# Kernel optimization log

Hardware: AMD Instinct MI355X
Metric: run time of the kernel (lower is better)

## Reference

```python
import jax, jax.numpy as jnp
import numpy as np

B, T, I, H = 64, 512, 512, 1024

def _xavier(key, shape):
    fan_in, fan_out = shape
    limit = float(np.sqrt(6.0 / (fan_in + fan_out)))
    return jax.random.uniform(key, shape, jnp.float32, -limit, limit)

def setup_inputs() -> dict:
    key = jax.random.key(0)
    ks = jax.random.split(key, 9)
    inp = {
        'x': jax.random.normal(ks[0], (B, T, I), jnp.float32),
        'U_inputgate': _xavier(ks[1], (I, H)),
        'V_inputgate': _xavier(ks[2], (H, H)),
        'bias_inputgate': jnp.zeros((H,), jnp.float32),
        'U_forget': _xavier(ks[3], (I, H)),
        'V_forget': _xavier(ks[4], (H, H)),
        'bias_forget': jnp.zeros((H,), jnp.float32),
        'U_tilded': _xavier(ks[5], (I, H)),
        'V_tilded': _xavier(ks[6], (H, H)),
        'bias_tilded': jnp.zeros((H,), jnp.float32),
        'U_output': _xavier(ks[7], (I, H)),
        'V_output': _xavier(ks[8], (H, H)),
        'bias_output': jnp.zeros((H,), jnp.float32),
    }
    return inp

def reference(x, U_inputgate, V_inputgate, bias_inputgate,
              U_forget, V_forget, bias_forget,
              U_tilded, V_tilded, bias_tilded,
              U_output, V_output, bias_output):
    batch = x.shape[0]
    hidden = V_inputgate.shape[0]
    # Precompute input projections for all timesteps (fused gate GEMM):
    # concat U's -> one [I, 4H] GEMM over the whole sequence.
    U = jnp.concatenate([U_inputgate, U_forget, U_tilded, U_output], axis=1)  # [I, 4H]
    V = jnp.concatenate([V_inputgate, V_forget, V_tilded, V_output], axis=1)  # [H, 4H]
    b = jnp.concatenate([bias_inputgate, bias_forget, bias_tilded, bias_output])  # [4H]
    xU = jnp.einsum('bti,ig->btg', x, U) + b  # [B, T, 4H]

    def step(carry, xu_t):
        h, c = carry
        g = xu_t + h @ V  # [B, 4H]
        i_g = jax.nn.sigmoid(g[:, :hidden])
        f_g = jax.nn.sigmoid(g[:, hidden:2 * hidden])
        c_t = jnp.tanh(g[:, 2 * hidden:3 * hidden])
        o_g = jax.nn.sigmoid(g[:, 3 * hidden:])
        c_new = i_g * c_t + f_g * c
        h_new = o_g * jnp.tanh(c_new)
        return (h_new, c_new), None

    h0 = jnp.zeros((batch, hidden), x.dtype)
    c0 = jnp.zeros((batch, hidden), x.dtype)
    (h_t, c_t), _ = jax.lax.scan(step, (h0, c0), jnp.swapaxes(xU, 0, 1))
    return (h_t, c_t)
```

## Files before the change

### kernel.cpp

```cpp
#include <hip/hip_runtime.h>
#include <hip/hip_bf16.h>
#include <cstdio>
#include <cstdint>

#define BB 64
#define TT 512
#define II 512
#define HH 1024
#define G4H 4096
#define TC 256

typedef __attribute__((ext_vector_type(8))) short short8b;
typedef __attribute__((ext_vector_type(4))) float f32x4;
typedef unsigned long long ull;

union U16 { uint4 u; short8b s; };

#define AT_LD32(p)   __hip_atomic_load((p), __ATOMIC_RELAXED, __HIP_MEMORY_SCOPE_AGENT)
#define AT_LD64(p)   __hip_atomic_load((p), __ATOMIC_RELAXED, __HIP_MEMORY_SCOPE_AGENT)
#define AT_ST32(p,v) __hip_atomic_store((p), (v), __ATOMIC_RELAXED, __HIP_MEMORY_SCOPE_AGENT)
#define AT_ST64(p,v) __hip_atomic_store((p), (v), __ATOMIC_RELAXED, __HIP_MEMORY_SCOPE_AGENT)

__device__ __forceinline__ ushort f2bf(float f) {
    union { float f; unsigned u; } x; x.f = f;
    unsigned r = x.u + 0x7FFFu + ((x.u >> 16) & 1u);
    return (ushort)(r >> 16);
}
__device__ __forceinline__ float bf2f(ushort b) {
    union { unsigned u; float f; } x; x.u = ((unsigned)b) << 16;
    return x.f;
}
__device__ __forceinline__ float sigm(float x) { return 1.f / (1.f + __expf(-x)); }
__device__ __forceinline__ float tanh_(float x) { return 2.f / (1.f + __expf(-2.f * x)) - 1.f; }

__global__ void conv_f32_bf16(const float* __restrict__ in, ushort* __restrict__ out, int n) {
    int i = (blockIdx.x * blockDim.x + threadIdx.x) * 4;
    int stride = gridDim.x * blockDim.x * 4;
    for (; i < n; i += stride) {
        float4 v = *(const float4*)(in + i);
        ushort4 o;
        o.x = f2bf(v.x); o.y = f2bf(v.y); o.z = f2bf(v.z); o.w = f2bf(v.w);
        *(ushort4*)(out + i) = o;
    }
}

__global__ void transpose_bf16(const float* __restrict__ in, ushort* __restrict__ out, int K) {
    __shared__ float tile[32][33];
    int j0 = blockIdx.x * 32;
    int k0 = blockIdx.y * 32;
    int tx = threadIdx.x, ty = threadIdx.y;
    #pragma unroll
    for (int i = 0; i < 32; i += 8)
        tile[ty + i][tx] = in[(size_t)(k0 + ty + i) * 1024 + j0 + tx];
    __syncthreads();
    #pragma unroll
    for (int i = 0; i < 32; i += 8)
        out[(size_t)(j0 + ty + i) * K + k0 + tx] = f2bf(tile[tx][ty + i]);
}

__global__ __launch_bounds__(256) void gemm_xu(
    const ushort* __restrict__ A, const ushort* __restrict__ Bt,
    const float* __restrict__ b0, const float* __restrict__ b1,
    const float* __restrict__ b2, const float* __restrict__ b3,
    ushort* __restrict__ C, int t0)
{
    __shared__ ushort As[128 * 64];
    __shared__ ushort Bs[128 * 64];
    const int m0 = blockIdx.x * 128;
    const int n0 = blockIdx.y * 128;
    const int tid = threadIdx.x;
    const int lane = tid & 63;
    const int wave = tid >> 6;
    const int wm = (wave >> 1) * 64;
    const int wn = (wave & 1) * 64;
    const int kgrp = lane >> 4;

    const ushort* Abase = A + ((size_t)(m0 >> 8) * TT + t0 + (m0 & 255)) * 512;

    f32x4 acc[4][4];
    #pragma unroll
    for (int i = 0; i < 4; ++i)
        #pragma unroll
        for (int j = 0; j < 4; ++j) acc[i][j] = (f32x4){0.f, 0.f, 0.f, 0.f};

    for (int k0 = 0; k0 < 512; k0 += 64) {
        __syncthreads();
        #pragma unroll
        for (int p = 0; p < 4; ++p) {
            int idx = p * 256 + tid;
            int row = idx >> 3;
            int kc  = idx & 7;
            uint4 va = *(const uint4*)(Abase + (size_t)row * 512 + k0 + kc * 8);
            uint4 vb = *(const uint4*)(Bt + (size_t)(n0 + row) * 512 + k0 + kc * 8);
            int bo = (row * 128 + kc * 16) ^ ((row & 7) << 4);
            *(uint4*)((char*)As + bo) = va;
            *(uint4*)((char*)Bs + bo) = vb;
        }
        __syncthreads();
        #pragma unroll
        for (int ks = 0; ks < 2; ++ks) {
            U16 af[4], bfr[4];
            #pragma unroll
            for (int i = 0; i < 4; ++i) {
                int row = wm + i * 16 + (lane & 15);
                int ao = (row * 128 + ks * 64 + kgrp * 16) ^ ((row & 7) << 4);
                af[i].u = *(const uint4*)((const char*)As + ao);
                int col = wn + i * 16 + (lane & 15);
                int bo = (col * 128 + ks * 64 + kgrp * 16) ^ ((col & 7) << 4);
                bfr[i].u = *(const uint4*)((const char*)Bs + bo);
            }
            #pragma unroll
            for (int i = 0; i < 4; ++i)
                #pragma unroll
                for (int j = 0; j < 4; ++j)
                    acc[i][j] = __builtin_amdgcn_mfma_f32_16x16x32_bf16(af[i].s, bfr[j].s, acc[i][j], 0, 0, 0);
        }
    }
    #pragma unroll
    for (int i = 0; i < 4; ++i) {
        #pragma unroll
        for (int j = 0; j < 4; ++j) {
            int row = m0 + wm + i * 16 + (lane >> 4) * 4;
            int col = n0 + wn + j * 16 + (lane & 15);
            int gate = col >> 10;
            const float* bp = (gate == 0) ? b0 : (gate == 1) ? b1 : (gate == 2) ? b2 : b3;
            float bias = bp[col & 1023];
            #pragma unroll
            for (int r = 0; r < 4; ++r)
                C[(size_t)(row + r) * G4H + col] = f2bf(acc[i][j][r] + bias);
        }
    }
}

__global__ __launch_bounds__(256) void lstm_rec(
    const ushort* __restrict__ xU,
    const ushort* __restrict__ V_t,
    ushort* __restrict__ hbuf,
    float* __restrict__ cbuf,
    float* __restrict__ out,
    unsigned* __restrict__ flags,
    int t0)
{
    __shared__ __align__(16) ushort Vl[64 * 1024];
    __shared__ __align__(16) ushort hl[16 * 1024];
    float* g_lds = (float*)hl;
    char* hb = (char*)hbuf;

    const int wgid = blockIdx.x;
    const int grp = wgid >> 6;
    const int slice = wgid & 63;
    const int tid = threadIdx.x;
    const int lane = tid & 63;
    const int gate = tid >> 6;

    #pragma unroll
    for (int p = 0; p < 32; ++p) {
        int idx = p * 256 + tid;
        int c  = idx >> 7;
        int kc = idx & 127;
        int colg = (c >> 4) * 1024 + slice * 16 + (c & 15);
        uint4 v = *(const uint4*)(V_t + (size_t)colg * 1024 + kc * 8);
        int bo = (c * 2048 + kc * 16) ^ ((c & 7) << 4);
        *(uint4*)((char*)Vl + bo) = v;
    }

    const int bb = tid >> 4, jh = tid & 15;
    const int hcol = slice * 16 + jh;
    const int growf = grp * 16 + bb;
    float c_reg;
    unsigned* myflag = flags + grp * 64 + slice;

    if (t0 == 0) {
        if (tid < 64)
            AT_ST64((ull*)(hb + grp * 32768 + slice * 512 + tid * 8), 0ull);
        c_reg = 0.f;
        __syncthreads();
        if (tid == 0) AT_ST32(myflag, 1u);
    } else {
        c_reg = cbuf[(size_t)growf * 1024 + hcol];
        __syncthreads();
    }

    const int kgrp = lane >> 4;
    const int lrow = lane & 15;
    const int arow_sw = (lrow & 7) << 4;
    const int bc = gate * 16 + (lane & 15);
    const int bxor = (bc & 7) << 4;
    const int bo_base = bc * 2048 + kgrp * 16;

    for (int t = t0; t < t0 + TC; ++t) {
        size_t xbase = ((size_t)growf * TC + (t - t0)) * G4H + hcol;
        ushort xi = xU[xbase], xf = xU[xbase + 1024], xc = xU[xbase + 2048], xo = xU[xbase + 3072];

        if (tid < 64) {
            unsigned tgt = (unsigned)(t + 1);
            const unsigned* f = flags + grp * 64;
            while (!__all((int)(AT_LD32(&f[tid]) >= tgt)))
                __builtin_amdgcn_s_sleep(1);
            asm volatile("" ::: "memory");
        }
        __syncthreads();

        {
            const char* hsrc = hb + (size_t)(t & 1) * 131072 + grp * 32768;
            ull vv[16];
            #pragma unroll
            for (int it = 0; it < 16; ++it) {
                int q = it * 256 + tid;
                vv[it] = AT_LD64((const ull*)(hsrc + (size_t)q * 8));
            }
            #pragma unroll
            for (int it = 0; it < 16; ++it) {
                int q = it * 256 + tid;
                int row = q >> 8;
                int cb  = (q & 255) * 8;
                *(ull*)((char*)hl + ((row * 2048 + cb) ^ ((row & 7) << 4))) = vv[it];
            }
        }
        __syncthreads();

        f32x4 acc0 = (f32x4){0.f,0.f,0.f,0.f}, acc1 = (f32x4){0.f,0.f,0.f,0.f};
        const char* hlb = (const char*)hl;
        #pragma unroll
        for (int ks = 0; ks < 32; ks += 2) {
            U16 a0, b0, a1, b1;
            a0.u = *(const uint4*)(hlb + ((lrow * 2048 + (ks * 4 + kgrp) * 16) ^ arow_sw));
            b0.u = *(const uint4*)((const char*)Vl + ((bo_base + ks * 64) ^ bxor));
            acc0 = __builtin_amdgcn_mfma_f32_16x16x32_bf16(a0.s, b0.s, acc0, 0, 0, 0);
            a1.u = *(const uint4*)(hlb + ((lrow * 2048 + (ks * 4 + 4 + kgrp) * 16) ^ arow_sw));
            b1.u = *(const uint4*)((const char*)Vl + ((bo_base + ks * 64 + 64) ^ bxor));
            acc1 = __builtin_amdgcn_mfma_f32_16x16x32_bf16(a1.s, b1.s, acc1, 0, 0, 0);
        }
        acc0 += acc1;
        __syncthreads();

        {
            int rb = (lane >> 4) * 4, col = gate * 16 + (lane & 15);
            #pragma unroll
            for (int r = 0; r < 4; ++r) g_lds[(rb + r) * 64 + col] = acc0[r];
        }
        __syncthreads();

        {
            float gi = g_lds[bb * 64 + jh]      + bf2f(xi);
            float gf = g_lds[bb * 64 + 16 + jh] + bf2f(xf);
            float gc = g_lds[bb * 64 + 32 + jh] + bf2f(xc);
            float go = g_lds[bb * 64 + 48 + jh] + bf2f(xo);
            float ig = sigm(gi), fg = sigm(gf), ct = tanh_(gc), og = sigm(go);
            c_reg = ig * ct + fg * c_reg;
            float h = og * tanh_(c_reg);
            ushort hbf = f2bf(h);
            unsigned v1 = __shfl_down((unsigned)hbf, 1);
            unsigned v2 = __shfl_down((unsigned)hbf, 2);
            unsigned v3 = __shfl_down((unsigned)hbf, 3);
            if ((jh & 3) == 0) {
                ull pk = (ull)((unsigned)hbf | (v1 << 16)) | (((ull)(v2 | (v3 << 16))) << 32);
                AT_ST64((ull*)(hb + (size_t)((t & 1) ^ 1) * 131072 + grp * 32768
                               + bb * 2048 + slice * 32 + jh * 2), pk);
            }
            if (t == TT - 1) {
                out[(size_t)growf * 1024 + hcol] = h;
                out[(size_t)BB * HH + (size_t)growf * 1024 + hcol] = c_reg;
            }
        }
        __syncthreads();
        if (tid == 0) AT_ST32(myflag, (unsigned)(t + 2));
    }

    if (t0 + TC < TT)
        cbuf[(size_t)growf * 1024 + hcol] = c_reg;
}

extern "C" void kernel_launch(void* const* d_in, const int* in_sizes, int n_in,
                              void* d_out, int out_size, void* d_ws, size_t ws_size,
                              hipStream_t stream) {
    const float* x = (const float*)d_in[0];
    const float* U[4] = {(const float*)d_in[1], (const float*)d_in[4], (const float*)d_in[7], (const float*)d_in[10]};
    const float* V[4] = {(const float*)d_in[2], (const float*)d_in[5], (const float*)d_in[8], (const float*)d_in[11]};
    const float* bias[4] = {(const float*)d_in[3], (const float*)d_in[6], (const float*)d_in[9], (const float*)d_in[12]};
    float* out = (float*)d_out;

    const size_t x_elems = (size_t)BB * TT * II;
    size_t off = 0;
    auto alloc = [&](size_t bytes) { size_t o = off; off = (off + bytes + 255) & ~(size_t)255; return o; };
    size_t o_xbf   = alloc(x_elems * 2);
    size_t o_Ut    = alloc((size_t)G4H * II * 2);
    size_t o_Vt    = alloc((size_t)G4H * HH * 2);
    size_t o_xU    = alloc((size_t)BB * TC * G4H * 2);
    size_t o_hbuf  = alloc((size_t)2 * BB * HH * 2);
    size_t o_cbuf  = alloc((size_t)BB * HH * 4);
    size_t o_flags = alloc(4 * 64 * 4);
    if (ws_size < off) {
        fprintf(stderr, "kernel_launch: ws too small: need %zu have %zu\n", off, ws_size);
        return;
    }
    char* ws = (char*)d_ws;
    ushort* x_bf = (ushort*)(ws + o_xbf);
    ushort* U_t  = (ushort*)(ws + o_Ut);
    ushort* V_t  = (ushort*)(ws + o_Vt);
    ushort* xU   = (ushort*)(ws + o_xU);
    ushort* hbuf = (ushort*)(ws + o_hbuf);
    float*  cbuf = (float*)(ws + o_cbuf);
    unsigned* flags = (unsigned*)(ws + o_flags);

    hipMemsetAsync(flags, 0, 4 * 64 * 4, stream);

    conv_f32_bf16<<<4096, 256, 0, stream>>>(x, x_bf, (int)x_elems);

    for (int g = 0; g < 4; ++g)
        transpose_bf16<<<dim3(32, 16), dim3(32, 8), 0, stream>>>(U[g], U_t + (size_t)g * 1024 * 512, 512);
    for (int g = 0; g < 4; ++g)
        transpose_bf16<<<dim3(32, 32), dim3(32, 8), 0, stream>>>(V[g], V_t + (size_t)g * 1024 * 1024, 1024);

    for (int c = 0; c < TT / TC; ++c) {
        int t0 = c * TC;
        gemm_xu<<<dim3(128, 32), 256, 0, stream>>>(x_bf, U_t, bias[0], bias[1], bias[2], bias[3], xU, t0);
        lstm_rec<<<256, 256, 0, stream>>>(xU, V_t, hbuf, cbuf, out, flags, t0);
    }
}
```

Baseline: 2.153 ms.

## Replace per-block flag barrier with epoch-tagged h packets for inter-block sync

The separate flag array and spin-wait barrier before reading h are removed. Each 64-bit store now carries three bf16 hidden values plus a 16-bit timestep tag, and readers poll their own packets until every tag matches the current step. This drops one round trip (flag store, flag poll, then data load) from the recurrent critical path per timestep. In exchange, each packet holds only 48 bits of payload, so there are more packets to load, the repacking into LDS is more complex, and the scheme relies on 64-bit stores landing atomically.

```diff
diff --git a/kernel.cpp b/kernel.cpp
--- a/kernel.cpp
+++ b/kernel.cpp
@@ -16,9 +16,7 @@
 
 union U16 { uint4 u; short8b s; };
 
-#define AT_LD32(p)   __hip_atomic_load((p), __ATOMIC_RELAXED, __HIP_MEMORY_SCOPE_AGENT)
 #define AT_LD64(p)   __hip_atomic_load((p), __ATOMIC_RELAXED, __HIP_MEMORY_SCOPE_AGENT)
-#define AT_ST32(p,v) __hip_atomic_store((p), (v), __ATOMIC_RELAXED, __HIP_MEMORY_SCOPE_AGENT)
 #define AT_ST64(p,v) __hip_atomic_store((p), (v), __ATOMIC_RELAXED, __HIP_MEMORY_SCOPE_AGENT)
 
 __device__ __forceinline__ ushort f2bf(float f) {
@@ -135,16 +133,14 @@
 __global__ __launch_bounds__(256) void lstm_rec(
     const ushort* __restrict__ xU,
     const ushort* __restrict__ V_t,
-    ushort* __restrict__ hbuf,
+    char* __restrict__ hb,
     float* __restrict__ cbuf,
     float* __restrict__ out,
-    unsigned* __restrict__ flags,
     int t0)
 {
     __shared__ __align__(16) ushort Vl[64 * 1024];
     __shared__ __align__(16) ushort hl[16 * 1024];
     float* g_lds = (float*)hl;
-    char* hb = (char*)hbuf;
 
     const int wgid = blockIdx.x;
     const int grp = wgid >> 6;
@@ -167,19 +163,7 @@
     const int bb = tid >> 4, jh = tid & 15;
     const int hcol = slice * 16 + jh;
     const int growf = grp * 16 + bb;
-    float c_reg;
-    unsigned* myflag = flags + grp * 64 + slice;
-
-    if (t0 == 0) {
-        if (tid < 64)
-            AT_ST64((ull*)(hb + grp * 32768 + slice * 512 + tid * 8), 0ull);
-        c_reg = 0.f;
-        __syncthreads();
-        if (tid == 0) AT_ST32(myflag, 1u);
-    } else {
-        c_reg = cbuf[(size_t)growf * 1024 + hcol];
-        __syncthreads();
-    }
+    float c_reg = (t0 == 0) ? 0.f : cbuf[(size_t)growf * 1024 + hcol];
 
     const int kgrp = lane >> 4;
     const int lrow = lane & 15;
@@ -188,33 +172,51 @@
     const int bxor = (bc & 7) << 4;
     const int bo_base = bc * 2048 + kgrp * 16;
 
+    const int pstrip = jh / 3;
+    const size_t pbyte = (size_t)grp * 49152 + (size_t)(pstrip * 1024 + slice * 16 + bb) * 8;
+
     for (int t = t0; t < t0 + TC; ++t) {
         size_t xbase = ((size_t)growf * TC + (t - t0)) * G4H + hcol;
         ushort xi = xU[xbase], xf = xU[xbase + 1024], xc = xU[xbase + 2048], xo = xU[xbase + 3072];
 
-        if (tid < 64) {
-            unsigned tgt = (unsigned)(t + 1);
-            const unsigned* f = flags + grp * 64;
-            while (!__all((int)(AT_LD32(&f[tid]) >= tgt)))
-                __builtin_amdgcn_s_sleep(1);
-            asm volatile("" ::: "memory");
-        }
-        __syncthreads();
-
+        ull pk[24];
         {
-            const char* hsrc = hb + (size_t)(t & 1) * 131072 + grp * 32768;
-            ull vv[16];
-            #pragma unroll
-            for (int it = 0; it < 16; ++it) {
-                int q = it * 256 + tid;
-                vv[it] = AT_LD64((const ull*)(hsrc + (size_t)q * 8));
-            }
-            #pragma unroll
-            for (int it = 0; it < 16; ++it) {
-                int q = it * 256 + tid;
-                int row = q >> 8;
-                int cb  = (q & 255) * 8;
-                *(ull*)((char*)hl + ((row * 2048 + cb) ^ ((row & 7) << 4))) = vv[it];
+            const char* pb = hb + (size_t)(t & 1) * 196608 + grp * 49152 + (size_t)tid * 8;
+            const ushort etag = (ushort)t;
+            unsigned mask = 0;
+            #pragma unroll
+            for (int i = 0; i < 24; ++i) pk[i] = AT_LD64((const ull*)(pb + i * 2048));
+            while (true) {
+                unsigned m = mask;
+                #pragma unroll
+                for (int i = 0; i < 24; ++i)
+                    if (!(m & (1u << i)) && (ushort)(pk[i] >> 48) == etag) m |= (1u << i);
+                mask = m;
+                if (mask == 0xFFFFFFu) break;
+                #pragma unroll
+                for (int i = 0; i < 24; ++i)
+                    if (!(mask & (1u << i))) pk[i] = AT_LD64((const ull*)(pb + i * 2048));
+            }
+        }
+        {
+            char* hp = (char*)hl;
+            #pragma unroll
+            for (int i = 0; i < 24; ++i) {
+                const int strip = i >> 2;
+                int sr = (i & 3) * 256 + tid;
+                int row = sr & 15;
+                int base = row * 2048 + (sr >> 4) * 32;
+                int xv = (row & 7) << 4;
+                unsigned v01 = (unsigned)(pk[i] & 0xffffffffu);
+                unsigned v12 = (unsigned)((pk[i] >> 16) & 0xffffffffu);
+                ushort v0 = (ushort)pk[i];
+                ushort v2 = (ushort)(pk[i] >> 32);
+                if (strip == 0) { *(unsigned*)(hp + ((base + 0) ^ xv)) = v01; *(ushort*)(hp + ((base + 4) ^ xv)) = v2; }
+                else if (strip == 1) { *(ushort*)(hp + ((base + 6) ^ xv)) = v0; *(unsigned*)(hp + ((base + 8) ^ xv)) = v12; }
+                else if (strip == 2) { *(unsigned*)(hp + ((base + 12) ^ xv)) = v01; *(ushort*)(hp + ((base + 16) ^ xv)) = v2; }
+                else if (strip == 3) { *(ushort*)(hp + ((base + 18) ^ xv)) = v0; *(unsigned*)(hp + ((base + 20) ^ xv)) = v12; }
+                else if (strip == 4) { *(unsigned*)(hp + ((base + 24) ^ xv)) = v01; *(ushort*)(hp + ((base + 28) ^ xv)) = v2; }
+                else { *(ushort*)(hp + ((base + 30) ^ xv)) = v0; }
             }
         }
         __syncthreads();
@@ -250,13 +252,12 @@
             c_reg = ig * ct + fg * c_reg;
             float h = og * tanh_(c_reg);
             ushort hbf = f2bf(h);
-            unsigned v1 = __shfl_down((unsigned)hbf, 1);
-            unsigned v2 = __shfl_down((unsigned)hbf, 2);
-            unsigned v3 = __shfl_down((unsigned)hbf, 3);
-            if ((jh & 3) == 0) {
-                ull pk = (ull)((unsigned)hbf | (v1 << 16)) | (((ull)(v2 | (v3 << 16))) << 32);
-                AT_ST64((ull*)(hb + (size_t)((t & 1) ^ 1) * 131072 + grp * 32768
-                               + bb * 2048 + slice * 32 + jh * 2), pk);
+            unsigned h1 = __shfl_down((unsigned)hbf, 1);
+            unsigned h2 = __shfl_down((unsigned)hbf, 2);
+            if (jh == pstrip * 3) {
+                ull pkt = (ull)hbf | ((ull)(h1 & 0xffff) << 16) | ((ull)(h2 & 0xffff) << 32)
+                        | ((ull)(ushort)(t + 1) << 48);
+                AT_ST64((ull*)(hb + (size_t)((t & 1) ^ 1) * 196608 + pbyte), pkt);
             }
             if (t == TT - 1) {
                 out[(size_t)growf * 1024 + hcol] = h;
@@ -264,7 +265,6 @@
             }
         }
         __syncthreads();
-        if (tid == 0) AT_ST32(myflag, (unsigned)(t + 2));
     }
 
     if (t0 + TC < TT)
@@ -287,9 +287,8 @@
     size_t o_Ut    = alloc((size_t)G4H * II * 2);
     size_t o_Vt    = alloc((size_t)G4H * HH * 2);
     size_t o_xU    = alloc((size_t)BB * TC * G4H * 2);
-    size_t o_hbuf  = alloc((size_t)2 * BB * HH * 2);
+    size_t o_hbuf  = alloc(2 * 4 * 6144 * 8);
     size_t o_cbuf  = alloc((size_t)BB * HH * 4);
-    size_t o_flags = alloc(4 * 64 * 4);
     if (ws_size < off) {
         fprintf(stderr, "kernel_launch: ws too small: need %zu have %zu\n", off, ws_size);
         return;
@@ -299,11 +298,10 @@
     ushort* U_t  = (ushort*)(ws + o_Ut);
     ushort* V_t  = (ushort*)(ws + o_Vt);
     ushort* xU   = (ushort*)(ws + o_xU);
-    ushort* hbuf = (ushort*)(ws + o_hbuf);
+    char*   hbuf = ws + o_hbuf;
     float*  cbuf = (float*)(ws + o_cbuf);
-    unsigned* flags = (unsigned*)(ws + o_flags);
-
-    hipMemsetAsync(flags, 0, 4 * 64 * 4, stream);
+
+    hipMemsetAsync(hbuf, 0, 2 * 4 * 6144 * 8, stream);
 
     conv_f32_bf16<<<4096, 256, 0, stream>>>(x, x_bf, (int)x_elems);
 
@@ -315,6 +313,6 @@
     for (int c = 0; c < TT / TC; ++c) {
         int t0 = c * TC;
         gemm_xu<<<dim3(128, 32), 256, 0, stream>>>(x_bf, U_t, bias[0], bias[1], bias[2], bias[3], xU, t0);
-        lstm_rec<<<256, 256, 0, stream>>>(xU, V_t, hbuf, cbuf, out, flags, t0);
-    }
-}
+        lstm_rec<<<256, 256, 0, stream>>>(xU, V_t, hbuf, cbuf, out, t0);
+    }
+}
```

Result: slower. 2.977 ms (+38.3%).

## Fold batch groups into each slice workgroup and pipeline per-group syncs

Applied to the files above, without the earlier changes.

The recurrent kernel now launches 64 workgroups, one per hidden slice, instead of 256. Each workgroup processes all four 16-row batch groups in turn inside every timestep, with a separate flag set per group. The point is that while one group waits on its cross-workgroup flags, the others can still make progress, and the grid-wide barrier traffic shrinks. The cost is four times more serial MFMA and gate work per workgroup on a quarter of the CUs, and h initialisation moves to a host-side memset.

```diff
diff --git a/kernel.cpp b/kernel.cpp
--- a/kernel.cpp
+++ b/kernel.cpp
@@ -9,6 +9,7 @@
 #define HH 1024
 #define G4H 4096
 #define TC 256
+#define NG 4
 
 typedef __attribute__((ext_vector_type(8))) short short8b;
 typedef __attribute__((ext_vector_type(4))) float f32x4;
@@ -135,7 +136,7 @@
 __global__ __launch_bounds__(256) void lstm_rec(
     const ushort* __restrict__ xU,
     const ushort* __restrict__ V_t,
-    ushort* __restrict__ hbuf,
+    char* __restrict__ hb,
     float* __restrict__ cbuf,
     float* __restrict__ out,
     unsigned* __restrict__ flags,
@@ -144,11 +145,8 @@
     __shared__ __align__(16) ushort Vl[64 * 1024];
     __shared__ __align__(16) ushort hl[16 * 1024];
     float* g_lds = (float*)hl;
-    char* hb = (char*)hbuf;
-
-    const int wgid = blockIdx.x;
-    const int grp = wgid >> 6;
-    const int slice = wgid & 63;
+
+    const int slice = blockIdx.x;
     const int tid = threadIdx.x;
     const int lane = tid & 63;
     const int gate = tid >> 6;
@@ -166,20 +164,10 @@
 
     const int bb = tid >> 4, jh = tid & 15;
     const int hcol = slice * 16 + jh;
-    const int growf = grp * 16 + bb;
-    float c_reg;
-    unsigned* myflag = flags + grp * 64 + slice;
-
-    if (t0 == 0) {
-        if (tid < 64)
-            AT_ST64((ull*)(hb + grp * 32768 + slice * 512 + tid * 8), 0ull);
-        c_reg = 0.f;
-        __syncthreads();
-        if (tid == 0) AT_ST32(myflag, 1u);
-    } else {
-        c_reg = cbuf[(size_t)growf * 1024 + hcol];
-        __syncthreads();
-    }
+    float c_reg[NG];
+    #pragma unroll
+    for (int g = 0; g < NG; ++g)
+        c_reg[g] = (t0 == 0) ? 0.f : cbuf[(size_t)(g * 16 + bb) * 1024 + hcol];
 
     const int kgrp = lane >> 4;
     const int lrow = lane & 15;
@@ -188,87 +176,99 @@
     const int bxor = (bc & 7) << 4;
     const int bo_base = bc * 2048 + kgrp * 16;
 
+    __syncthreads();
+
     for (int t = t0; t < t0 + TC; ++t) {
-        size_t xbase = ((size_t)growf * TC + (t - t0)) * G4H + hcol;
-        ushort xi = xU[xbase], xf = xU[xbase + 1024], xc = xU[xbase + 2048], xo = xU[xbase + 3072];
-
-        if (tid < 64) {
-            unsigned tgt = (unsigned)(t + 1);
-            const unsigned* f = flags + grp * 64;
-            while (!__all((int)(AT_LD32(&f[tid]) >= tgt)))
-                __builtin_amdgcn_s_sleep(1);
-            asm volatile("" ::: "memory");
-        }
-        __syncthreads();
-
-        {
-            const char* hsrc = hb + (size_t)(t & 1) * 131072 + grp * 32768;
-            ull vv[16];
+        ushort xg[NG][4];
+        #pragma unroll
+        for (int g = 0; g < NG; ++g) {
+            size_t xb = ((size_t)(g * 16 + bb) * TC + (t - t0)) * G4H + hcol;
+            xg[g][0] = xU[xb];        xg[g][1] = xU[xb + 1024];
+            xg[g][2] = xU[xb + 2048]; xg[g][3] = xU[xb + 3072];
+        }
+
+        #pragma unroll
+        for (int g = 0; g < NG; ++g) {
+            if (tid < 64) {
+                const unsigned tgt = (unsigned)t;
+                const unsigned* f = flags + g * 64;
+                while (AT_LD32(&f[tid]) < tgt)
+                    __builtin_amdgcn_s_sleep(1);
+                asm volatile("" ::: "memory");
+            }
+            __syncthreads();
+
+            {
+                const char* hsrc = hb + (size_t)(t & 1) * 131072 + g * 32768;
+                ull vv[16];
+                #pragma unroll
+                for (int it = 0; it < 16; ++it)
+                    vv[it] = AT_LD64((const ull*)(hsrc + (size_t)(it * 256 + tid) * 8));
+                #pragma unroll
+                for (int it = 0; it < 16; ++it) {
+                    int q = it * 256 + tid;
+                    int row = q >> 8;
+                    int cb  = (q & 255) * 8;
+                    *(ull*)((char*)hl + ((row * 2048 + cb) ^ ((row & 7) << 4))) = vv[it];
+                }
+            }
+            __syncthreads();
+
+            f32x4 acc0 = (f32x4){0.f,0.f,0.f,0.f}, acc1 = (f32x4){0.f,0.f,0.f,0.f};
+            const char* hlb = (const char*)hl;
             #pragma unroll
-            for (int it = 0; it < 16; ++it) {
-                int q = it * 256 + tid;
-                vv[it] = AT_LD64((const ull*)(hsrc + (size_t)q * 8));
-            }
-            #pragma unroll
-            for (int it = 0; it < 16; ++it) {
-                int q = it * 256 + tid;
-                int row = q >> 8;
-                int cb  = (q & 255) * 8;
-                *(ull*)((char*)hl + ((row * 2048 + cb) ^ ((row & 7) << 4))) = vv[it];
-            }
-        }
-        __syncthreads();
-
-        f32x4 acc0 = (f32x4){0.f,0.f,0.f,0.f}, acc1 = (f32x4){0.f,0.f,0.f,0.f};
-        const char* hlb = (const char*)hl;
-        #pragma unroll
-        for (int ks = 0; ks < 32; ks += 2) {
-            U16 a0, b0, a1, b1;
-            a0.u = *(const uint4*)(hlb + ((lrow * 2048 + (ks * 4 + kgrp) * 16) ^ arow_sw));
-            b0.u = *(const uint4*)((const char*)Vl + ((bo_base + ks * 64) ^ bxor));
-            acc0 = __builtin_amdgcn_mfma_f32_16x16x32_bf16(a0.s, b0.s, acc0, 0, 0, 0);
-            a1.u = *(const uint4*)(hlb + ((lrow * 2048 + (ks * 4 + 4 + kgrp) * 16) ^ arow_sw));
-            b1.u = *(const uint4*)((const char*)Vl + ((bo_base + ks * 64 + 64) ^ bxor));
-            acc1 = __builtin_amdgcn_mfma_f32_16x16x32_bf16(a1.s, b1.s, acc1, 0, 0, 0);
-        }
-        acc0 += acc1;
-        __syncthreads();
-
-        {
-            int rb = (lane >> 4) * 4, col = gate * 16 + (lane & 15);
-            #pragma unroll
-            for (int r = 0; r < 4; ++r) g_lds[(rb + r) * 64 + col] = acc0[r];
-        }
-        __syncthreads();
-
-        {
-            float gi = g_lds[bb * 64 + jh]      + bf2f(xi);
-            float gf = g_lds[bb * 64 + 16 + jh] + bf2f(xf);
-            float gc = g_lds[bb * 64 + 32 + jh] + bf2f(xc);
-            float go = g_lds[bb * 64 + 48 + jh] + bf2f(xo);
-            float ig = sigm(gi), fg = sigm(gf), ct = tanh_(gc), og = sigm(go);
-            c_reg = ig * ct + fg * c_reg;
-            float h = og * tanh_(c_reg);
-            ushort hbf = f2bf(h);
-            unsigned v1 = __shfl_down((unsigned)hbf, 1);
-            unsigned v2 = __shfl_down((unsigned)hbf, 2);
-            unsigned v3 = __shfl_down((unsigned)hbf, 3);
-            if ((jh & 3) == 0) {
-                ull pk = (ull)((unsigned)hbf | (v1 << 16)) | (((ull)(v2 | (v3 << 16))) << 32);
-                AT_ST64((ull*)(hb + (size_t)((t & 1) ^ 1) * 131072 + grp * 32768
-                               + bb * 2048 + slice * 32 + jh * 2), pk);
-            }
-            if (t == TT - 1) {
-                out[(size_t)growf * 1024 + hcol] = h;
-                out[(size_t)BB * HH + (size_t)growf * 1024 + hcol] = c_reg;
-            }
-        }
-        __syncthreads();
-        if (tid == 0) AT_ST32(myflag, (unsigned)(t + 2));
-    }
-
-    if (t0 + TC < TT)
-        cbuf[(size_t)growf * 1024 + hcol] = c_reg;
+            for (int ks = 0; ks < 32; ks += 2) {
+                U16 a0, b0, a1, b1;
+                a0.u = *(const uint4*)(hlb + ((lrow * 2048 + (ks * 4 + kgrp) * 16) ^ arow_sw));
+                b0.u = *(const uint4*)((const char*)Vl + ((bo_base + ks * 64) ^ bxor));
+                acc0 = __builtin_amdgcn_mfma_f32_16x16x32_bf16(a0.s, b0.s, acc0, 0, 0, 0);
+                a1.u = *(const uint4*)(hlb + ((lrow * 2048 + (ks * 4 + 4 + kgrp) * 16) ^ arow_sw));
+                b1.u = *(const uint4*)((const char*)Vl + ((bo_base + ks * 64 + 64) ^ bxor));
+                acc1 = __builtin_amdgcn_mfma_f32_16x16x32_bf16(a1.s, b1.s, acc1, 0, 0, 0);
+            }
+            acc0 += acc1;
+            __syncthreads();
+
+            {
+                int rb = (lane >> 4) * 4, col = gate * 16 + (lane & 15);
+                #pragma unroll
+                for (int r = 0; r < 4; ++r) g_lds[(rb + r) * 64 + col] = acc0[r];
+            }
+            __syncthreads();
+
+            {
+                float gi = g_lds[bb * 64 + jh]      + bf2f(xg[g][0]);
+                float gf = g_lds[bb * 64 + 16 + jh] + bf2f(xg[g][1]);
+                float gc = g_lds[bb * 64 + 32 + jh] + bf2f(xg[g][2]);
+                float go = g_lds[bb * 64 + 48 + jh] + bf2f(xg[g][3]);
+                float ig = sigm(gi), fg = sigm(gf), ct = tanh_(gc), og = sigm(go);
+                c_reg[g] = ig * ct + fg * c_reg[g];
+                float h = og * tanh_(c_reg[g]);
+                ushort hbf = f2bf(h);
+                unsigned h1 = __shfl_down((unsigned)hbf, 1);
+                unsigned h2 = __shfl_down((unsigned)hbf, 2);
+                unsigned h3 = __shfl_down((unsigned)hbf, 3);
+                if ((jh & 3) == 0) {
+                    ull pk = (ull)hbf | ((ull)(h1 & 0xffff) << 16)
+                           | ((ull)(h2 & 0xffff) << 32) | ((ull)(h3 & 0xffff) << 48);
+                    AT_ST64((ull*)(hb + (size_t)((t & 1) ^ 1) * 131072 + g * 32768
+                                   + bb * 2048 + (size_t)(slice * 16 + jh) * 2), pk);
+                }
+                if (t == TT - 1) {
+                    out[(size_t)(g * 16 + bb) * 1024 + hcol] = h;
+                    out[(size_t)BB * HH + (size_t)(g * 16 + bb) * 1024 + hcol] = c_reg[g];
+                }
+            }
+            __syncthreads();
+            if (tid == 0) AT_ST32(flags + g * 64 + slice, (unsigned)(t + 1));
+        }
+    }
+
+    if (t0 + TC < TT) {
+        #pragma unroll
+        for (int g = 0; g < NG; ++g)
+            cbuf[(size_t)(g * 16 + bb) * 1024 + hcol] = c_reg[g];
+    }
 }
 
 extern "C" void kernel_launch(void* const* d_in, const int* in_sizes, int n_in,
@@ -287,9 +287,9 @@
     size_t o_Ut    = alloc((size_t)G4H * II * 2);
     size_t o_Vt    = alloc((size_t)G4H * HH * 2);
     size_t o_xU    = alloc((size_t)BB * TC * G4H * 2);
-    size_t o_hbuf  = alloc((size_t)2 * BB * HH * 2);
+    size_t o_hbuf  = alloc(262144);
     size_t o_cbuf  = alloc((size_t)BB * HH * 4);
-    size_t o_flags = alloc(4 * 64 * 4);
+    size_t o_flags = alloc(NG * 64 * 4);
     if (ws_size < off) {
         fprintf(stderr, "kernel_launch: ws too small: need %zu have %zu\n", off, ws_size);
         return;
@@ -299,11 +299,12 @@
     ushort* U_t  = (ushort*)(ws + o_Ut);
     ushort* V_t  = (ushort*)(ws + o_Vt);
     ushort* xU   = (ushort*)(ws + o_xU);
-    ushort* hbuf = (ushort*)(ws + o_hbuf);
+    char*   hbuf = ws + o_hbuf;
     float*  cbuf = (float*)(ws + o_cbuf);
     unsigned* flags = (unsigned*)(ws + o_flags);
 
-    hipMemsetAsync(flags, 0, 4 * 64 * 4, stream);
+    hipMemsetAsync(flags, 0, NG * 64 * 4, stream);
+    hipMemsetAsync(hbuf, 0, 262144, stream);
 
     conv_f32_bf16<<<4096, 256, 0, stream>>>(x, x_bf, (int)x_elems);
 
@@ -315,6 +316,6 @@
     for (int c = 0; c < TT / TC; ++c) {
         int t0 = c * TC;
         gemm_xu<<<dim3(128, 32), 256, 0, stream>>>(x_bf, U_t, bias[0], bias[1], bias[2], bias[3], xU, t0);
-        lstm_rec<<<256, 256, 0, stream>>>(xU, V_t, hbuf, cbuf, out, flags, t0);
-    }
-}
+        lstm_rec<<<64, 256, 0, stream>>>(xU, V_t, hbuf, cbuf, out, flags, t0);
+    }
+}
```

Measured after the change: 5.579 ms. +159.1%, slower.

## Load h directly from global into registers and drop per-step LDS staging barriers

Applied to the files above, without the earlier changes.

The recurrent kernel no longer stages the shared h state through LDS. Each wave spins on the flags itself and loads its MFMA A-operand fragments straight from global memory into 64 registers. The gate scratch is double-buffered by timestep, which removes two of the four block barriers per step, and h is zero-initialised with a host memset instead of an in-kernel init. This cuts barrier and LDS round-trip latency on the serial critical path. In exchange every wave issues redundant global loads and register pressure rises.

```diff
diff --git a/kernel.cpp b/kernel.cpp
--- a/kernel.cpp
+++ b/kernel.cpp
@@ -132,19 +132,17 @@
     }
 }
 
-__global__ __launch_bounds__(256) void lstm_rec(
+__global__ __launch_bounds__(256, 1) void lstm_rec(
     const ushort* __restrict__ xU,
     const ushort* __restrict__ V_t,
-    ushort* __restrict__ hbuf,
+    char* __restrict__ hb,
     float* __restrict__ cbuf,
     float* __restrict__ out,
     unsigned* __restrict__ flags,
     int t0)
 {
     __shared__ __align__(16) ushort Vl[64 * 1024];
-    __shared__ __align__(16) ushort hl[16 * 1024];
-    float* g_lds = (float*)hl;
-    char* hb = (char*)hbuf;
+    __shared__ float g_lds[2][16][64];
 
     const int wgid = blockIdx.x;
     const int grp = wgid >> 6;
@@ -167,96 +165,76 @@
     const int bb = tid >> 4, jh = tid & 15;
     const int hcol = slice * 16 + jh;
     const int growf = grp * 16 + bb;
-    float c_reg;
-    unsigned* myflag = flags + grp * 64 + slice;
-
-    if (t0 == 0) {
-        if (tid < 64)
-            AT_ST64((ull*)(hb + grp * 32768 + slice * 512 + tid * 8), 0ull);
-        c_reg = 0.f;
-        __syncthreads();
-        if (tid == 0) AT_ST32(myflag, 1u);
-    } else {
-        c_reg = cbuf[(size_t)growf * 1024 + hcol];
-        __syncthreads();
-    }
+    float c_reg = (t0 == 0) ? 0.f : cbuf[(size_t)growf * 1024 + hcol];
 
     const int kgrp = lane >> 4;
     const int lrow = lane & 15;
-    const int arow_sw = (lrow & 7) << 4;
     const int bc = gate * 16 + (lane & 15);
     const int bxor = (bc & 7) << 4;
     const int bo_base = bc * 2048 + kgrp * 16;
 
+    __syncthreads();
+
     for (int t = t0; t < t0 + TC; ++t) {
         size_t xbase = ((size_t)growf * TC + (t - t0)) * G4H + hcol;
         ushort xi = xU[xbase], xf = xU[xbase + 1024], xc = xU[xbase + 2048], xo = xU[xbase + 3072];
 
-        if (tid < 64) {
-            unsigned tgt = (unsigned)(t + 1);
+        {
+            const unsigned tgt = (unsigned)t;
             const unsigned* f = flags + grp * 64;
-            while (!__all((int)(AT_LD32(&f[tid]) >= tgt)))
+            while (!__all((int)(AT_LD32(&f[lane]) >= tgt)))
                 __builtin_amdgcn_s_sleep(1);
             asm volatile("" ::: "memory");
         }
-        __syncthreads();
-
-        {
-            const char* hsrc = hb + (size_t)(t & 1) * 131072 + grp * 32768;
-            ull vv[16];
-            #pragma unroll
-            for (int it = 0; it < 16; ++it) {
-                int q = it * 256 + tid;
-                vv[it] = AT_LD64((const ull*)(hsrc + (size_t)q * 8));
-            }
-            #pragma unroll
-            for (int it = 0; it < 16; ++it) {
-                int q = it * 256 + tid;
-                int row = q >> 8;
-                int cb  = (q & 255) * 8;
-                *(ull*)((char*)hl + ((row * 2048 + cb) ^ ((row & 7) << 4))) = vv[it];
-            }
-        }
-        __syncthreads();
+
+        ull A8[64];
+        {
+            const char* hsrc = hb + (size_t)(t & 1) * 131072 + grp * 32768
+                             + lrow * 2048 + kgrp * 16;
+            #pragma unroll
+            for (int q = 0; q < 64; ++q)
+                A8[q] = AT_LD64((const ull*)(hsrc + (q >> 1) * 64 + (q & 1) * 8));
+        }
 
         f32x4 acc0 = (f32x4){0.f,0.f,0.f,0.f}, acc1 = (f32x4){0.f,0.f,0.f,0.f};
-        const char* hlb = (const char*)hl;
         #pragma unroll
         for (int ks = 0; ks < 32; ks += 2) {
             U16 a0, b0, a1, b1;
-            a0.u = *(const uint4*)(hlb + ((lrow * 2048 + (ks * 4 + kgrp) * 16) ^ arow_sw));
+            a0.u.x = (unsigned)A8[2 * ks];     a0.u.y = (unsigned)(A8[2 * ks] >> 32);
+            a0.u.z = (unsigned)A8[2 * ks + 1]; a0.u.w = (unsigned)(A8[2 * ks + 1] >> 32);
             b0.u = *(const uint4*)((const char*)Vl + ((bo_base + ks * 64) ^ bxor));
             acc0 = __builtin_amdgcn_mfma_f32_16x16x32_bf16(a0.s, b0.s, acc0, 0, 0, 0);
-            a1.u = *(const uint4*)(hlb + ((lrow * 2048 + (ks * 4 + 4 + kgrp) * 16) ^ arow_sw));
+            a1.u.x = (unsigned)A8[2 * ks + 2]; a1.u.y = (unsigned)(A8[2 * ks + 2] >> 32);
+            a1.u.z = (unsigned)A8[2 * ks + 3]; a1.u.w = (unsigned)(A8[2 * ks + 3] >> 32);
             b1.u = *(const uint4*)((const char*)Vl + ((bo_base + ks * 64 + 64) ^ bxor));
             acc1 = __builtin_amdgcn_mfma_f32_16x16x32_bf16(a1.s, b1.s, acc1, 0, 0, 0);
         }
         acc0 += acc1;
-        __syncthreads();
 
         {
             int rb = (lane >> 4) * 4, col = gate * 16 + (lane & 15);
             #pragma unroll
-            for (int r = 0; r < 4; ++r) g_lds[(rb + r) * 64 + col] = acc0[r];
-        }
-        __syncthreads();
-
-        {
-            float gi = g_lds[bb * 64 + jh]      + bf2f(xi);
-            float gf = g_lds[bb * 64 + 16 + jh] + bf2f(xf);
-            float gc = g_lds[bb * 64 + 32 + jh] + bf2f(xc);
-            float go = g_lds[bb * 64 + 48 + jh] + bf2f(xo);
+            for (int r = 0; r < 4; ++r) g_lds[t & 1][rb + r][col] = acc0[r];
+        }
+        __syncthreads();
+
+        {
+            float gi = g_lds[t & 1][bb][jh]      + bf2f(xi);
+            float gf = g_lds[t & 1][bb][16 + jh] + bf2f(xf);
+            float gc = g_lds[t & 1][bb][32 + jh] + bf2f(xc);
+            float go = g_lds[t & 1][bb][48 + jh] + bf2f(xo);
             float ig = sigm(gi), fg = sigm(gf), ct = tanh_(gc), og = sigm(go);
             c_reg = ig * ct + fg * c_reg;
             float h = og * tanh_(c_reg);
             ushort hbf = f2bf(h);
-            unsigned v1 = __shfl_down((unsigned)hbf, 1);
-            unsigned v2 = __shfl_down((unsigned)hbf, 2);
-            unsigned v3 = __shfl_down((unsigned)hbf, 3);
+            unsigned h1 = __shfl_down((unsigned)hbf, 1);
+            unsigned h2 = __shfl_down((unsigned)hbf, 2);
+            unsigned h3 = __shfl_down((unsigned)hbf, 3);
             if ((jh & 3) == 0) {
-                ull pk = (ull)((unsigned)hbf | (v1 << 16)) | (((ull)(v2 | (v3 << 16))) << 32);
+                ull pk = (ull)hbf | ((ull)(h1 & 0xffff) << 16)
+                       | ((ull)(h2 & 0xffff) << 32) | ((ull)(h3 & 0xffff) << 48);
                 AT_ST64((ull*)(hb + (size_t)((t & 1) ^ 1) * 131072 + grp * 32768
-                               + bb * 2048 + slice * 32 + jh * 2), pk);
+                               + bb * 2048 + (size_t)(slice * 16 + jh) * 2), pk);
             }
             if (t == TT - 1) {
                 out[(size_t)growf * 1024 + hcol] = h;
@@ -264,7 +242,7 @@
             }
         }
         __syncthreads();
-        if (tid == 0) AT_ST32(myflag, (unsigned)(t + 2));
+        if (tid == 0) AT_ST32(flags + grp * 64 + slice, (unsigned)(t + 1));
     }
 
     if (t0 + TC < TT)
@@ -287,7 +265,7 @@
     size_t o_Ut    = alloc((size_t)G4H * II * 2);
     size_t o_Vt    = alloc((size_t)G4H * HH * 2);
     size_t o_xU    = alloc((size_t)BB * TC * G4H * 2);
-    size_t o_hbuf  = alloc((size_t)2 * BB * HH * 2);
+    size_t o_hbuf  = alloc(262144);
     size_t o_cbuf  = alloc((size_t)BB * HH * 4);
     size_t o_flags = alloc(4 * 64 * 4);
     if (ws_size < off) {
@@ -299,11 +277,12 @@
     ushort* U_t  = (ushort*)(ws + o_Ut);
     ushort* V_t  = (ushort*)(ws + o_Vt);
     ushort* xU   = (ushort*)(ws + o_xU);
-    ushort* hbuf = (ushort*)(ws + o_hbuf);
+    char*   hbuf = ws + o_hbuf;
     float*  cbuf = (float*)(ws + o_cbuf);
     unsigned* flags = (unsigned*)(ws + o_flags);
 
     hipMemsetAsync(flags, 0, 4 * 64 * 4, stream);
+    hipMemsetAsync(hbuf, 0, 262144, stream);
 
     conv_f32_bf16<<<4096, 256, 0, stream>>>(x, x_bf, (int)x_elems);
 
```

Result: slower. 5.226 ms (+142.7%).
